# Kernel tuning notes

Hardware: AMD Instinct MI355X
Metric: run time of the kernel (lower is better)

## Reference

```python
import jax, jax.numpy as jnp
import numpy as np


def cayley_batch(data):
    # data: (b, r, r). Q = (I + skew) @ (I - skew)^{-1}  (torch solve with left=False)
    b, rr, _ = data.shape
    skew = 0.5 * (data - data.transpose(0, 2, 1))
    I = jnp.eye(rr, dtype=data.dtype)
    A = I - skew  # always invertible (skew-symmetric)
    B = I + skew
    # Solve X @ A = B  ->  A^T X^T = B^T
    Q = jnp.linalg.solve(A.transpose(0, 2, 1), B.transpose(0, 2, 1)).transpose(0, 2, 1)
    return Q


def blockdiag_butterfly_multiply(x, w1, w2):
    # x: (batch, n); w1: (k, q, p) with k*p == n; w2: (l, s, r) with l*r == k*q
    batch = x.shape[0]
    k, q, p = w1.shape
    l, s, r = w2.shape
    out1 = jnp.einsum('bkp,kqp->bkq', x.reshape(batch, k, p), w1)  # (batch, k, q)
    # flat (k*q) viewed as (r, l), then transposed -> (batch, l, r)
    out1 = out1.reshape(batch, r, l).transpose(0, 2, 1)
    out2 = jnp.einsum('blr,lsr->bls', out1, w2)  # (batch, l, s)
    # permute to (batch, s, l) and flatten -> (batch, s*l)
    return out2.transpose(0, 2, 1).reshape(batch, s * l)


def setup_inputs() -> dict:
    key = jax.random.key(0)
    k1, k2, k3 = jax.random.split(key, 3)
    n, nblocks = 4096, 64
    bs = n // nblocks  # 64
    x = jax.random.normal(k1, (16384, n), dtype=jnp.float32)
    L = jax.random.normal(k2, (nblocks, bs, bs), dtype=jnp.float32)
    R = jax.random.normal(k3, (nblocks, bs, bs), dtype=jnp.float32)
    return {"x": x, "L": L, "R": R}


def reference(x, L, R):
    # GSOrthogonal.forward with orthogonal=True, method='cayley':
    # orthogonalize L and R, then butterfly multiply with (x, R_orth, L_orth)
    Lq = cayley_batch(L)
    Rq = cayley_batch(R)
    return blockdiag_butterfly_multiply(x, Rq, Lq)
```

## Files before the change

kernel.cpp:

```cpp
#include <hip/hip_runtime.h>
#include <hip/hip_bf16.h>

typedef __bf16 bf16x4 __attribute__((ext_vector_type(4)));
typedef __bf16 bf16x8 __attribute__((ext_vector_type(8)));
typedef float  floatx4 __attribute__((ext_vector_type(4)));

__global__ __launch_bounds__(256) void cayley_pack_kernel(
    const float* __restrict__ L, const float* __restrict__ R,
    __bf16* __restrict__ ws) {
  __shared__ float Ms[64][65];
  __shared__ float Pa[64];
  __shared__ float Pi[64];
  __shared__ float fcol[2][64];

  const int blk = blockIdx.x;
  const int t = threadIdx.x;
  const float* M = (blk < 64) ? (R + (size_t)blk * 4096)
                              : (L + (size_t)(blk - 64) * 4096);
  __bf16* dst = ws + (size_t)blk * 4096;

  for (int u = 0; u < 16; ++u) {
    int idx = u * 256 + t;
    Ms[idx >> 6][idx & 63] = M[idx];
  }
  __syncthreads();

  const int i = t >> 2;
  const int g = t & 3;
  const int jb = g * 16;
  float a[16], v[16];
#pragma unroll
  for (int jj = 0; jj < 16; ++jj) {
    int j = jb + jj;
    float s = 0.5f * (Ms[i][j] - Ms[j][i]);
    a[jj] = (i == j ? 1.0f : 0.0f) - s;
    v[jj] = (i == j ? 1.0f : 0.0f);
  }
  __syncthreads();

#pragma unroll
  for (int k = 0; k < 64; ++k) {
    if (g == (k >> 4)) fcol[k & 1][i] = a[k & 15];
    __syncthreads();
    if (i == k) {
      float ip = 1.0f / fcol[k & 1][k];
#pragma unroll
      for (int jj = 0; jj < 16; ++jj) {
        a[jj] *= ip; v[jj] *= ip;
        Pa[jb + jj] = a[jj]; Pi[jb + jj] = v[jj];
      }
    }
    __syncthreads();
    if (i != k) {
      float f = fcol[k & 1][i];
#pragma unroll
      for (int jj = 0; jj < 16; ++jj) {
        a[jj] -= f * Pa[jb + jj];
        v[jj] -= f * Pi[jb + jj];
      }
    }
  }

#pragma unroll
  for (int jj = 0; jj < 16; ++jj) {
    int j = jb + jj;
    Ms[i][j] = 2.0f * v[jj] - (i == j ? 1.0f : 0.0f);
  }
  __syncthreads();

  const int lane = t & 63;
  const int grp = t >> 6;
  const int colq = lane & 15;
  const int quad = lane >> 4;
#pragma unroll
  for (int kh = 0; kh < 2; ++kh) {
    bf16x8 pk;
#pragma unroll
    for (int j8 = 0; j8 < 8; ++j8)
      pk[j8] = (__bf16)Ms[16 * grp + colq][32 * kh + 8 * quad + j8];
    *(bf16x8*)(dst + (kh * 4 + grp) * 512 + lane * 8) = pk;
  }
}

__global__ __launch_bounds__(256, 2) void butterfly_kernel(
    const float* __restrict__ x, const __bf16* __restrict__ ws,
    float* __restrict__ out) {
  __shared__ short interS[32768];
  __bf16* inter = (__bf16*)interS;

  const int t = threadIdx.x;
  const int wv = t >> 6;
  const int lane = t & 63;
  const int col = lane & 15;
  const int quad = lane >> 4;
  const size_t b0 = (size_t)blockIdx.x * 8;

  const __bf16* w1 = ws;
  const __bf16* w2 = ws + 64 * 4096;

  const float* xrow = x + (b0 + (size_t)(col & 7)) * 4096;
#pragma unroll
  for (int rg = 0; rg < 4; ++rg) {
    const int r0 = wv * 16 + rg * 4;
    bf16x8 afrag[4][2];
#pragma unroll
    for (int ir = 0; ir < 4; ++ir) {
      const float* src = xrow + (r0 + ir) * 64 + quad * 8;
#pragma unroll
      for (int kh = 0; kh < 2; ++kh) {
        floatx4 u = *(const floatx4*)(src + kh * 32);
        floatx4 w = *(const floatx4*)(src + kh * 32 + 4);
        bf16x8 f;
        f[0] = (__bf16)u[0]; f[1] = (__bf16)u[1];
        f[2] = (__bf16)u[2]; f[3] = (__bf16)u[3];
        f[4] = (__bf16)w[0]; f[5] = (__bf16)w[1];
        f[6] = (__bf16)w[2]; f[7] = (__bf16)w[3];
        afrag[ir][kh] = f;
      }
    }
#pragma unroll
    for (int qc = 0; qc < 4; ++qc) {
      floatx4 vals[4];
#pragma unroll
      for (int ir = 0; ir < 4; ++ir) {
        const int r = r0 + ir;
        bf16x8 bf0 = *(const bf16x8*)(w1 + (size_t)r * 4096 + (0 * 4 + qc) * 512 + lane * 8);
        bf16x8 bf1 = *(const bf16x8*)(w1 + (size_t)r * 4096 + (1 * 4 + qc) * 512 + lane * 8);
        floatx4 acc = {0.f, 0.f, 0.f, 0.f};
        acc = __builtin_amdgcn_mfma_f32_16x16x32_bf16(afrag[ir][0], bf0, acc, 0, 0, 0);
        acc = __builtin_amdgcn_mfma_f32_16x16x32_bf16(afrag[ir][1], bf1, acc, 0, 0, 0);
        vals[ir] = acc;
      }
      if (quad < 2) {
        const int l = qc * 16 + col;
        const int c = r0 >> 3;
        const int ls = l & 7;
#pragma unroll
        for (int reg = 0; reg < 4; ++reg) {
          const int b = quad * 4 + reg;
          bf16x4 pk;
          pk[0] = (__bf16)vals[0][reg];
          pk[1] = (__bf16)vals[1][reg];
          pk[2] = (__bf16)vals[2][reg];
          pk[3] = (__bf16)vals[3][reg];
          const int cs = c ^ b ^ ls;
          *(bf16x4*)(inter + l * 512 + b * 64 + cs * 8 + (r0 & 7)) = pk;
        }
      }
    }
  }
  __syncthreads();

  const int b = col & 7;
  float* outb = out + b0 * 4096;
#pragma unroll
  for (int sc = 0; sc < 4; ++sc) {
    floatx4 vals[16];
#pragma unroll
    for (int l16 = 0; l16 < 16; ++l16) {
      const int l = wv * 16 + l16;
      const int swz = b ^ (l & 7);
      bf16x8 a0 = *(const bf16x8*)(inter + l * 512 + b * 64 + (quad ^ swz) * 8);
      bf16x8 a1 = *(const bf16x8*)(inter + l * 512 + b * 64 + ((4 + quad) ^ swz) * 8);
      bf16x8 bf0 = *(const bf16x8*)(w2 + (size_t)l * 4096 + (0 * 4 + sc) * 512 + lane * 8);
      bf16x8 bf1 = *(const bf16x8*)(w2 + (size_t)l * 4096 + (1 * 4 + sc) * 512 + lane * 8);
      floatx4 acc = {0.f, 0.f, 0.f, 0.f};
      acc = __builtin_amdgcn_mfma_f32_16x16x32_bf16(a0, bf0, acc, 0, 0, 0);
      acc = __builtin_amdgcn_mfma_f32_16x16x32_bf16(a1, bf1, acc, 0, 0, 0);
      vals[l16] = acc;
    }
    if (quad < 2) {
      const int s = sc * 16 + col;
#pragma unroll
      for (int reg = 0; reg < 4; ++reg) {
        const int bb = quad * 4 + reg;
        float* dstp = outb + (size_t)bb * 4096 + s * 64 + wv * 16;
#pragma unroll
        for (int q4 = 0; q4 < 4; ++q4) {
          floatx4 vv;
          vv[0] = vals[q4 * 4 + 0][reg];
          vv[1] = vals[q4 * 4 + 1][reg];
          vv[2] = vals[q4 * 4 + 2][reg];
          vv[3] = vals[q4 * 4 + 3][reg];
          *(floatx4*)(dstp + q4 * 4) = vv;
        }
      }
    }
  }
}

extern "C" void kernel_launch(void* const* d_in, const int* in_sizes, int n_in,
                              void* d_out, int out_size, void* d_ws, size_t ws_size,
                              hipStream_t stream) {
  const float* x = (const float*)d_in[0];
  const float* L = (const float*)d_in[1];
  const float* R = (const float*)d_in[2];
  float* out = (float*)d_out;
  __bf16* ws = (__bf16*)d_ws;

  const int nrows = in_sizes[0] / 4096;

  cayley_pack_kernel<<<128, 256, 0, stream>>>(L, R, ws);
  butterfly_kernel<<<nrows / 8, 256, 0, stream>>>(x, ws, out);
}
```

Measured before the change: 570.6 us.

## Process 16 rows per block in four l-chunk phases with smaller LDS

The butterfly kernel now handles 16 batch rows per block, which fills every MFMA row instead of wasting half the lanes. It splits the work into four phases, each computing a 16-column slice of the first GEMM and then the matching 16 l-blocks of the second GEMM, so the LDS intermediate shrinks to 32KB and occupancy can rise to 4 blocks per CU. In exchange it adds two barriers per phase and rereads the x rows from global memory in every phase, four times in total, which depends on cache hits to stay cheap.

```diff
diff --git a/kernel.cpp b/kernel.cpp
--- a/kernel.cpp
+++ b/kernel.cpp
@@ -82,108 +82,103 @@
   }
 }
 
-__global__ __launch_bounds__(256, 2) void butterfly_kernel(
+__global__ __launch_bounds__(256, 4) void butterfly_kernel(
     const float* __restrict__ x, const __bf16* __restrict__ ws,
     float* __restrict__ out) {
-  __shared__ short interS[32768];
-  __bf16* inter = (__bf16*)interS;
+  __shared__ __bf16 inter[16 * 1024];
 
   const int t = threadIdx.x;
   const int wv = t >> 6;
   const int lane = t & 63;
   const int col = lane & 15;
   const int quad = lane >> 4;
-  const size_t b0 = (size_t)blockIdx.x * 8;
+  const size_t b0 = (size_t)blockIdx.x * 16;
 
   const __bf16* w1 = ws;
   const __bf16* w2 = ws + 64 * 4096;
 
-  const float* xrow = x + (b0 + (size_t)(col & 7)) * 4096;
-#pragma unroll
-  for (int rg = 0; rg < 4; ++rg) {
-    const int r0 = wv * 16 + rg * 4;
-    bf16x8 afrag[4][2];
-#pragma unroll
-    for (int ir = 0; ir < 4; ++ir) {
-      const float* src = xrow + (r0 + ir) * 64 + quad * 8;
-#pragma unroll
-      for (int kh = 0; kh < 2; ++kh) {
-        floatx4 u = *(const floatx4*)(src + kh * 32);
-        floatx4 w = *(const floatx4*)(src + kh * 32 + 4);
-        bf16x8 f;
-        f[0] = (__bf16)u[0]; f[1] = (__bf16)u[1];
-        f[2] = (__bf16)u[2]; f[3] = (__bf16)u[3];
-        f[4] = (__bf16)w[0]; f[5] = (__bf16)w[1];
-        f[6] = (__bf16)w[2]; f[7] = (__bf16)w[3];
-        afrag[ir][kh] = f;
-      }
-    }
-#pragma unroll
-    for (int qc = 0; qc < 4; ++qc) {
+  const float* xrow = x + (b0 + (size_t)col) * 4096;
+  float* outb = out + b0 * 4096;
+
+  for (int p = 0; p < 4; ++p) {
+#pragma unroll
+    for (int rg = 0; rg < 4; ++rg) {
+      const int r0 = wv * 16 + rg * 4;
       floatx4 vals[4];
 #pragma unroll
       for (int ir = 0; ir < 4; ++ir) {
         const int r = r0 + ir;
-        bf16x8 bf0 = *(const bf16x8*)(w1 + (size_t)r * 4096 + (0 * 4 + qc) * 512 + lane * 8);
-        bf16x8 bf1 = *(const bf16x8*)(w1 + (size_t)r * 4096 + (1 * 4 + qc) * 512 + lane * 8);
+        const float* src = xrow + r * 64 + quad * 8;
+        bf16x8 af[2];
+#pragma unroll
+        for (int kh = 0; kh < 2; ++kh) {
+          floatx4 u = *(const floatx4*)(src + kh * 32);
+          floatx4 w = *(const floatx4*)(src + kh * 32 + 4);
+          bf16x8 f;
+          f[0] = (__bf16)u[0]; f[1] = (__bf16)u[1];
+          f[2] = (__bf16)u[2]; f[3] = (__bf16)u[3];
+          f[4] = (__bf16)w[0]; f[5] = (__bf16)w[1];
+          f[6] = (__bf16)w[2]; f[7] = (__bf16)w[3];
+          af[kh] = f;
+        }
+        bf16x8 bf0 = *(const bf16x8*)(w1 + (size_t)r * 4096 + (0 * 4 + p) * 512 + lane * 8);
+        bf16x8 bf1 = *(const bf16x8*)(w1 + (size_t)r * 4096 + (1 * 4 + p) * 512 + lane * 8);
         floatx4 acc = {0.f, 0.f, 0.f, 0.f};
-        acc = __builtin_amdgcn_mfma_f32_16x16x32_bf16(afrag[ir][0], bf0, acc, 0, 0, 0);
-        acc = __builtin_amdgcn_mfma_f32_16x16x32_bf16(afrag[ir][1], bf1, acc, 0, 0, 0);
+        acc = __builtin_amdgcn_mfma_f32_16x16x32_bf16(af[0], bf0, acc, 0, 0, 0);
+        acc = __builtin_amdgcn_mfma_f32_16x16x32_bf16(af[1], bf1, acc, 0, 0, 0);
         vals[ir] = acc;
       }
-      if (quad < 2) {
-        const int l = qc * 16 + col;
-        const int c = r0 >> 3;
-        const int ls = l & 7;
-#pragma unroll
-        for (int reg = 0; reg < 4; ++reg) {
-          const int b = quad * 4 + reg;
-          bf16x4 pk;
-          pk[0] = (__bf16)vals[0][reg];
-          pk[1] = (__bf16)vals[1][reg];
-          pk[2] = (__bf16)vals[2][reg];
-          pk[3] = (__bf16)vals[3][reg];
-          const int cs = c ^ b ^ ls;
-          *(bf16x4*)(inter + l * 512 + b * 64 + cs * 8 + (r0 & 7)) = pk;
-        }
-      }
-    }
-  }
-  __syncthreads();
-
-  const int b = col & 7;
-  float* outb = out + b0 * 4096;
-#pragma unroll
-  for (int sc = 0; sc < 4; ++sc) {
-    floatx4 vals[16];
-#pragma unroll
-    for (int l16 = 0; l16 < 16; ++l16) {
-      const int l = wv * 16 + l16;
-      const int swz = b ^ (l & 7);
-      bf16x8 a0 = *(const bf16x8*)(inter + l * 512 + b * 64 + (quad ^ swz) * 8);
-      bf16x8 a1 = *(const bf16x8*)(inter + l * 512 + b * 64 + ((4 + quad) ^ swz) * 8);
-      bf16x8 bf0 = *(const bf16x8*)(w2 + (size_t)l * 4096 + (0 * 4 + sc) * 512 + lane * 8);
-      bf16x8 bf1 = *(const bf16x8*)(w2 + (size_t)l * 4096 + (1 * 4 + sc) * 512 + lane * 8);
-      floatx4 acc = {0.f, 0.f, 0.f, 0.f};
-      acc = __builtin_amdgcn_mfma_f32_16x16x32_bf16(a0, bf0, acc, 0, 0, 0);
-      acc = __builtin_amdgcn_mfma_f32_16x16x32_bf16(a1, bf1, acc, 0, 0, 0);
-      vals[l16] = acc;
-    }
-    if (quad < 2) {
+      const int c = r0 >> 3;
+      const int off = r0 & 7;
+#pragma unroll
+      for (int reg = 0; reg < 4; ++reg) {
+        const int b = quad * 4 + reg;
+        bf16x4 pk;
+        pk[0] = (__bf16)vals[0][reg];
+        pk[1] = (__bf16)vals[1][reg];
+        pk[2] = (__bf16)vals[2][reg];
+        pk[3] = (__bf16)vals[3][reg];
+        const int ch = c ^ (b & 7) ^ (col & 7);
+        *(bf16x4*)(&inter[col * 1024 + b * 64 + ch * 8 + off]) = pk;
+      }
+    }
+    __syncthreads();
+
+    bf16x8 afr[4][2];
+#pragma unroll
+    for (int l4 = 0; l4 < 4; ++l4) {
+      const int ll = wv * 4 + l4;
+#pragma unroll
+      for (int kh = 0; kh < 2; ++kh) {
+        const int ch = (kh * 4 + quad) ^ (col & 7) ^ (ll & 7);
+        afr[l4][kh] = *(const bf16x8*)(&inter[ll * 1024 + col * 64 + ch * 8]);
+      }
+    }
+    __syncthreads();
+
+#pragma unroll
+    for (int sc = 0; sc < 4; ++sc) {
+      floatx4 acc[4];
+#pragma unroll
+      for (int l4 = 0; l4 < 4; ++l4) {
+        const int l = p * 16 + wv * 4 + l4;
+        bf16x8 bf0 = *(const bf16x8*)(w2 + (size_t)l * 4096 + (0 * 4 + sc) * 512 + lane * 8);
+        bf16x8 bf1 = *(const bf16x8*)(w2 + (size_t)l * 4096 + (1 * 4 + sc) * 512 + lane * 8);
+        floatx4 a = {0.f, 0.f, 0.f, 0.f};
+        a = __builtin_amdgcn_mfma_f32_16x16x32_bf16(afr[l4][0], bf0, a, 0, 0, 0);
+        a = __builtin_amdgcn_mfma_f32_16x16x32_bf16(afr[l4][1], bf1, a, 0, 0, 0);
+        acc[l4] = a;
+      }
       const int s = sc * 16 + col;
 #pragma unroll
       for (int reg = 0; reg < 4; ++reg) {
-        const int bb = quad * 4 + reg;
-        float* dstp = outb + (size_t)bb * 4096 + s * 64 + wv * 16;
-#pragma unroll
-        for (int q4 = 0; q4 < 4; ++q4) {
-          floatx4 vv;
-          vv[0] = vals[q4 * 4 + 0][reg];
-          vv[1] = vals[q4 * 4 + 1][reg];
-          vv[2] = vals[q4 * 4 + 2][reg];
-          vv[3] = vals[q4 * 4 + 3][reg];
-          *(floatx4*)(dstp + q4 * 4) = vv;
-        }
+        const int bq = quad * 4 + reg;
+        floatx4 vv;
+        vv[0] = acc[0][reg];
+        vv[1] = acc[1][reg];
+        vv[2] = acc[2][reg];
+        vv[3] = acc[3][reg];
+        *(floatx4*)(outb + (size_t)bq * 4096 + s * 64 + p * 16 + wv * 4) = vv;
       }
     }
   }
@@ -201,5 +196,5 @@
   const int nrows = in_sizes[0] / 4096;
 
   cayley_pack_kernel<<<128, 256, 0, stream>>>(L, R, ws);
-  butterfly_kernel<<<nrows / 8, 256, 0, stream>>>(x, ws, out);
+  butterfly_kernel<<<nrows / 16, 256, 0, stream>>>(x, ws, out);
 }
```

Measured after the change: 712.7 us. 24.9% more time.
